# Kernel optimization log

Hardware: AMD Instinct MI355X
Metric: run time of the kernel (lower is better)

Reference implementation:

```python
import jax, jax.numpy as jnp
import numpy as np

NUM_CLASSES = 256
FEATURE_DIM = 768
BATCH = 128
SIM_BALANCE = 0.7
TIER1 = 50.0
TIER2 = 10.0
TOPK = 5


def _l2norm(x):
    return x / jnp.linalg.norm(x, axis=1, keepdims=True)


def build_edge_weights(class_features, context_features, w1, b1, w2, b2,
                       co_occurrence, instance_counts):
    """Vectorized, faithful translation of VisualFeatureGraph.build_graph."""
    N = class_features.shape[0]
    dt = class_features.dtype
    co = co_occurrence.astype(dt)            # [N,N], diag is 0
    cnt = instance_counts.astype(dt)         # [N]

    vs = _l2norm(class_features) @ _l2norm(class_features).T    # visual_sim [N,N]
    cs = _l2norm(context_features) @ _l2norm(context_features).T  # context_sim
    combined = SIM_BALANCE * vs + (1.0 - SIM_BALANCE) * cs

    # ---- Tier 1: co > TIER1 ----
    # sim_proj(f_i - f_j): exploit linearity of first layer: (f_i-f_j)@W1 = a_i - a_j
    a = class_features @ w1                                    # [N, D/2]
    h = jax.nn.relu(a[:, None, :] - a[None, :, :] + b1)        # [N,N,D/2]
    sim_weight = jax.nn.sigmoid(h @ w2 + b2)[..., 0]           # [N,N]
    ratio = (jnp.minimum(cnt[:, None], cnt[None, :]) /
             jnp.maximum(jnp.maximum(cnt[:, None], cnt[None, :]), 1.0))
    e1 = combined * sim_weight * ratio

    # ---- Tier 2: TIER2 < co <= TIER1 ----
    # shared neighbors k: co[i,k]>T1 and co[j,k]>T1 (k=i,j auto-excluded: diag=0
    # and co[i,j]<=T1 for tier-2 pairs)
    A = (co > TIER1).astype(dt)                                # [N,N]
    M = vs * A
    shared_sum = M @ M.T                                       # sum_k vs[i,k]*vs[j,k]
    shared_cnt = A @ A.T
    avg_sim = shared_sum / jnp.maximum(shared_cnt, 1.0)
    conf = co / TIER1
    e2 = jnp.where(shared_cnt > 0,
                   conf * combined + (1.0 - conf) * avg_sim,
                   conf * combined)

    # ---- Tier 3: co <= TIER2 ----
    # top-5 neighbors per row by co-occurrence among co > TIER2 (diag=0 and
    # co[i,j]<=TIER2 for tier-3 pairs, so i and j are auto-excluded)
    top_vals, top_idx = jax.lax.top_k(co, TOPK)                # [N,K]
    valid = top_vals > TIER2                                   # [N,K]
    ii = top_idx[:, None, :, None]                             # [N,1,K,1]
    jj = top_idx[None, :, None, :]                             # [1,N,1,K]
    co_cross = co[ii, jj]                                      # co[i_neigh, j_neigh] [N,N,K,K]
    vs_cross = vs[ii, jj]
    vs_in = jnp.take_along_axis(vs, top_idx, axis=1)           # vs[i, i_neigh] [N,K]
    mask = valid[:, None, :, None] & valid[None, :, None, :] & (co_cross > 0)
    w = (top_vals[:, None, :, None] * top_vals[None, :, None, :]) / TIER1
    w = jnp.where(mask, w, 0.0)
    sim = vs_in[:, None, :, None] * vs_in[None, :, None, :] * vs_cross
    trans = jnp.sum(w * sim, axis=(2, 3))                      # [N,N]
    tot = jnp.sum(w, axis=(2, 3))
    e3 = jnp.where(tot > 0, trans / jnp.where(tot > 0, tot, 1.0), 0.1 * cs)

    tier1_mask = co > TIER1
    tier2_mask = (co > TIER2) & ~tier1_mask
    E = jnp.where(tier1_mask, e1, jnp.where(tier2_mask, e2, e3))
    E = E * (1.0 - jnp.eye(N, dtype=dt))                       # i==j skipped
    mx = jnp.max(E)
    E = jnp.where(mx > 0, E / jnp.where(mx > 0, mx, 1.0), E)
    return E


def setup_inputs() -> dict:
    key = jax.random.key(0)
    ks = jax.random.split(key, 8)
    N, D, B = NUM_CLASSES, FEATURE_DIM, BATCH
    x = jax.random.normal(ks[0], (B, N, D), dtype=jnp.float32)
    class_features = jax.random.normal(ks[1], (N, D), dtype=jnp.float32) * 0.05
    context_features = jax.random.normal(ks[2], (N, D), dtype=jnp.float32) * 0.05
    w1 = jax.random.normal(ks[3], (D, D // 2), dtype=jnp.float32) * (1.0 / np.sqrt(D))
    b1 = jnp.zeros((D // 2,), dtype=jnp.float32)
    w2 = jax.random.normal(ks[4], (D // 2, 1), dtype=jnp.float32) * (1.0 / np.sqrt(D // 2))
    b2 = jnp.zeros((1,), dtype=jnp.float32)
    co = jax.random.randint(ks[5], (N, N), 0, 121, dtype=jnp.int32)
    co = (co + co.T) // 2                                      # symmetric like update_features
    co = co * (1 - jnp.eye(N, dtype=jnp.int32))                # zero diagonal
    instance_counts = jax.random.randint(ks[6], (N,), 1, 1001, dtype=jnp.int32)
    return {"x": x, "class_features": class_features,
            "context_features": context_features,
            "w1": w1, "b1": b1, "w2": w2, "b2": b2,
            "co_occurrence": co, "instance_counts": instance_counts}


def reference(x, class_features, context_features, w1, b1, w2, b2,
              co_occurrence, instance_counts):
    E = build_edge_weights(class_features, context_features, w1, b1, w2, b2,
                           co_occurrence, instance_counts)
    # torch.bmm(E.expand(B,-1,-1), x) == einsum over shared node dim
    return x + jnp.einsum('ij,bjd->bid', E, x)
```

## Files before the change

### kernel.cpp

```cpp
#include <hip/hip_runtime.h>
#include <hip/hip_bf16.h>
#include <math.h>

#define N 256
#define D 768
#define BATCH 128

typedef float f32x4 __attribute__((ext_vector_type(4)));
typedef short bf16x8 __attribute__((ext_vector_type(8)));

static __device__ __forceinline__ unsigned short f2bf(float f) {
    unsigned int u = __float_as_uint(f);
    u += 0x7fffu + ((u >> 16) & 1u);
    return (unsigned short)(u >> 16);
}
static __device__ __forceinline__ unsigned int pack2bf(float lo, float hi) {
    unsigned int a = __float_as_uint(lo);
    unsigned int b = __float_as_uint(hi);
    a += 0x7fffu + ((a >> 16) & 1u);
    b += 0x7fffu + ((b >> 16) & 1u);
    return (a >> 16) | (b & 0xffff0000u);
}

__global__ void k_stage1(const float* __restrict__ cf, const float* __restrict__ ctx,
                         float* __restrict__ vsn, float* __restrict__ csn,
                         const float* __restrict__ w1, float* __restrict__ a,
                         const int* __restrict__ co, float* __restrict__ topv,
                         int* __restrict__ topi) {
    __shared__ float sm[2 * 64 * 33];
    int bx = blockIdx.x;
    int t = threadIdx.x;
    if (bx < 512) {
        int row = bx;
        const float* src;
        float* dst;
        if (row < N) { src = cf  + row * D;       dst = vsn + row * D; }
        else         { src = ctx + (row - N) * D; dst = csn + (row - N) * D; }
        float s = 0.f;
        for (int d = t; d < D; d += 256) { float v = src[d]; s += v * v; }
        float* red = sm;
        red[t] = s; __syncthreads();
        for (int off = 128; off > 0; off >>= 1) {
            if (t < off) red[t] += red[t + off];
            __syncthreads();
        }
        float inv = 1.0f / sqrtf(red[0]);
        for (int d = t; d < D; d += 256) dst[d] = src[d] * inv;
    } else if (bx < 608) {
        int bi = bx - 512;
        int i0 = (bi / 12) * 32, j0 = (bi % 12) * 32;
        float (*Ci)[33] = (float(*)[33])sm;
        float (*Wj)[33] = (float(*)[33])(sm + 64 * 33);
        int tx = t & 15, ty = t >> 4;
        float a00 = 0.f, a01 = 0.f, a10 = 0.f, a11 = 0.f;
        for (int k0 = 0; k0 < 768; k0 += 64) {
            #pragma unroll
            for (int s = 0; s < 8; s++) {
                int idx = s * 256 + t;
                int row = idx >> 6, kc = idx & 63;
                Ci[kc][row] = cf[(i0 + row) * 768 + k0 + kc];
                int kr = idx >> 5, col = idx & 31;
                Wj[kr][col] = w1[(k0 + kr) * 384 + j0 + col];
            }
            __syncthreads();
            #pragma unroll 4
            for (int kk = 0; kk < 64; kk++) {
                float iv0 = Ci[kk][ty * 2], iv1 = Ci[kk][ty * 2 + 1];
                float jv0 = Wj[kk][tx * 2], jv1 = Wj[kk][tx * 2 + 1];
                a00 += iv0 * jv0; a01 += iv0 * jv1;
                a10 += iv1 * jv0; a11 += iv1 * jv1;
            }
            __syncthreads();
        }
        a[(i0 + ty * 2)     * 384 + j0 + tx * 2]     = a00;
        a[(i0 + ty * 2)     * 384 + j0 + tx * 2 + 1] = a01;
        a[(i0 + ty * 2 + 1) * 384 + j0 + tx * 2]     = a10;
        a[(i0 + ty * 2 + 1) * 384 + j0 + tx * 2 + 1] = a11;
    } else {
        int lane = t & 63;
        int row = (bx - 608) * 4 + (t >> 6);
        int4 v4 = *(const int4*)(co + row * 256 + lane * 4);
        int key[4];
        key[0] = v4.x * 256 + (255 - (lane * 4 + 0));
        key[1] = v4.y * 256 + (255 - (lane * 4 + 1));
        key[2] = v4.z * 256 + (255 - (lane * 4 + 2));
        key[3] = v4.w * 256 + (255 - (lane * 4 + 3));
        for (int r = 0; r < 5; r++) {
            int best = key[0];
            #pragma unroll
            for (int e = 1; e < 4; e++) best = max(best, key[e]);
            #pragma unroll
            for (int off = 32; off > 0; off >>= 1) best = max(best, __shfl_xor(best, off, 64));
            int kidx = 255 - (best & 255);
            int val = best >> 8;
            if (lane == 0) { topv[row * 5 + r] = (float)val; topi[row * 5 + r] = kidx; }
            if ((kidx >> 2) == lane) key[kidx & 3] = -1;
        }
    }
}

__global__ void k_gram2(const float* __restrict__ vsn, const float* __restrict__ csn,
                        float* __restrict__ vs, float* __restrict__ cs) {
    int bx = blockIdx.x;
    const float* S = (bx >= 64) ? csn : vsn;
    float* O       = (bx >= 64) ? cs  : vs;
    int bi = bx & 63;
    int i0 = (bi >> 3) * 32, j0 = (bi & 7) * 32;
    __shared__ float Li[64][33], Lj[64][33];
    int t = threadIdx.x;
    int tx = t & 15, ty = t >> 4;
    float a00 = 0.f, a01 = 0.f, a10 = 0.f, a11 = 0.f;
    for (int k0 = 0; k0 < 768; k0 += 64) {
        #pragma unroll
        for (int s = 0; s < 8; s++) {
            int idx = s * 256 + t;
            int row = idx >> 6, kc = idx & 63;
            Li[kc][row] = S[(i0 + row) * 768 + k0 + kc];
            Lj[kc][row] = S[(j0 + row) * 768 + k0 + kc];
        }
        __syncthreads();
        #pragma unroll 4
        for (int kk = 0; kk < 64; kk++) {
            float iv0 = Li[kk][ty * 2], iv1 = Li[kk][ty * 2 + 1];
            float jv0 = Lj[kk][tx * 2], jv1 = Lj[kk][tx * 2 + 1];
            a00 += iv0 * jv0; a01 += iv0 * jv1;
            a10 += iv1 * jv0; a11 += iv1 * jv1;
        }
        __syncthreads();
    }
    O[(i0 + ty * 2)     * 256 + j0 + tx * 2]     = a00;
    O[(i0 + ty * 2)     * 256 + j0 + tx * 2 + 1] = a01;
    O[(i0 + ty * 2 + 1) * 256 + j0 + tx * 2]     = a10;
    O[(i0 + ty * 2 + 1) * 256 + j0 + tx * 2 + 1] = a11;
}

__global__ void k_stage3(const float* __restrict__ a, const float* __restrict__ b1,
                         const float* __restrict__ w2, const float* __restrict__ b2,
                         const float* __restrict__ vs, const float* __restrict__ cs,
                         const int* __restrict__ ic, float* __restrict__ e1,
                         const int* __restrict__ co, float* __restrict__ ss,
                         float* __restrict__ sc) {
    __shared__ float sm[12800];
    int bx = blockIdx.x;
    int t = threadIdx.x;
    if (bx < 256) {
        int i0 = (bx >> 4) * 16, j0 = (bx & 15) * 16;
        float (*ai)[388]  = (float(*)[388])sm;
        float (*ajm)[388] = (float(*)[388])(sm + 16 * 388);
        float* sw2 = sm + 2 * 16 * 388;
        for (int idx = t; idx < 16 * 96; idx += 256) {
            int r = idx / 96, c = (idx % 96) * 4;
            *(float4*)&ai[r][c] = *(const float4*)(a + (i0 + r) * 384 + c);
            float4 u  = *(const float4*)(a + (j0 + r) * 384 + c);
            float4 bb = *(const float4*)(b1 + c);
            u.x -= bb.x; u.y -= bb.y; u.z -= bb.z; u.w -= bb.w;
            *(float4*)&ajm[r][c] = u;
        }
        for (int k = t; k < 384; k += 256) sw2[k] = w2[k];
        __syncthreads();
        int tx = t & 15, ty = t >> 4;
        float s = 0.f;
        #pragma unroll 4
        for (int k4 = 0; k4 < 96; k4++) {
            float4 xv = *(const float4*)&ai[ty][k4 * 4];
            float4 yv = *(const float4*)&ajm[tx][k4 * 4];
            float4 wv = *(const float4*)&sw2[k4 * 4];
            s += fmaxf(xv.x - yv.x, 0.f) * wv.x;
            s += fmaxf(xv.y - yv.y, 0.f) * wv.y;
            s += fmaxf(xv.z - yv.z, 0.f) * wv.z;
            s += fmaxf(xv.w - yv.w, 0.f) * wv.w;
        }
        int i = i0 + ty, j = j0 + tx;
        float sig = 1.0f / (1.0f + expf(-(s + b2[0])));
        float comb = 0.7f * vs[i * 256 + j] + 0.3f * cs[i * 256 + j];
        float ci = (float)ic[i], cj = (float)ic[j];
        float mn = fminf(ci, cj), mx = fmaxf(ci, cj);
        float ratio = mn / fmaxf(mx, 1.0f);
        e1[i * 256 + j] = comb * sig * ratio;
    } else {
        int bi = bx - 256;
        int i0 = (bi >> 3) * 32, j0 = (bi & 7) * 32;
        float (*Mi)[33] = (float(*)[33])sm;
        float (*Ai)[33] = (float(*)[33])(sm + 2112);
        float (*Mj)[33] = (float(*)[33])(sm + 4224);
        float (*Aj)[33] = (float(*)[33])(sm + 6336);
        int tx = t & 15, ty = t >> 4;
        float s00=0.f,s01=0.f,s10=0.f,s11=0.f;
        float c00=0.f,c01=0.f,c10=0.f,c11=0.f;
        for (int k0 = 0; k0 < 256; k0 += 64) {
            #pragma unroll
            for (int s = 0; s < 8; s++) {
                int idx = s * 256 + t;
                int row = idx >> 6, kc = idx & 63;
                int civ = co[(i0 + row) * 256 + k0 + kc];
                float aa = civ > 50 ? 1.f : 0.f;
                Ai[kc][row] = aa;
                Mi[kc][row] = aa * vs[(i0 + row) * 256 + k0 + kc];
                int cjv = co[(j0 + row) * 256 + k0 + kc];
                float ab = cjv > 50 ? 1.f : 0.f;
                Aj[kc][row] = ab;
                Mj[kc][row] = ab * vs[(j0 + row) * 256 + k0 + kc];
            }
            __syncthreads();
            #pragma unroll 4
            for (int kk = 0; kk < 64; kk++) {
                float mi0 = Mi[kk][ty*2], mi1 = Mi[kk][ty*2+1];
                float ai0 = Ai[kk][ty*2], ai1 = Ai[kk][ty*2+1];
                float mj0 = Mj[kk][tx*2], mj1 = Mj[kk][tx*2+1];
                float aj0 = Aj[kk][tx*2], aj1 = Aj[kk][tx*2+1];
                s00 += mi0*mj0; s01 += mi0*mj1; s10 += mi1*mj0; s11 += mi1*mj1;
                c00 += ai0*aj0; c01 += ai0*aj1; c10 += ai1*aj0; c11 += ai1*aj1;
            }
            __syncthreads();
        }
        ss[(i0+ty*2)  *256 + j0+tx*2]   = s00; ss[(i0+ty*2)  *256 + j0+tx*2+1] = s01;
        ss[(i0+ty*2+1)*256 + j0+tx*2]   = s10; ss[(i0+ty*2+1)*256 + j0+tx*2+1] = s11;
        sc[(i0+ty*2)  *256 + j0+tx*2]   = c00; sc[(i0+ty*2)  *256 + j0+tx*2+1] = c01;
        sc[(i0+ty*2+1)*256 + j0+tx*2]   = c10; sc[(i0+ty*2+1)*256 + j0+tx*2+1] = c11;
    }
}

__global__ void k_assemble(const int* __restrict__ co, const float* __restrict__ vs,
                           const float* __restrict__ cs, const float* __restrict__ e1,
                           const float* __restrict__ ss, const float* __restrict__ sc,
                           const float* __restrict__ topv, const int* __restrict__ topi,
                           float* __restrict__ E, float* __restrict__ partials) {
    int i = blockIdx.x, j = threadIdx.x;
    int cij = co[i * 256 + j];
    float e;
    if (i == j) {
        e = 0.f;
    } else if (cij > 50) {
        e = e1[i * 256 + j];
    } else if (cij > 10) {
        float conf = (float)cij / 50.0f;
        float comb = 0.7f * vs[i * 256 + j] + 0.3f * cs[i * 256 + j];
        float cnt = sc[i * 256 + j];
        float avg = ss[i * 256 + j] / fmaxf(cnt, 1.f);
        e = (cnt > 0.f) ? conf * comb + (1.f - conf) * avg : conf * comb;
    } else {
        float tvi[5], tvj[5]; int tii[5], tij[5];
        #pragma unroll
        for (int k = 0; k < 5; k++) {
            tvi[k] = topv[i * 5 + k]; tii[k] = topi[i * 5 + k];
            tvj[k] = topv[j * 5 + k]; tij[k] = topi[j * 5 + k];
        }
        float trans = 0.f, tot = 0.f;
        #pragma unroll
        for (int k = 0; k < 5; k++) {
            if (!(tvi[k] > 10.f)) continue;
            float vin_i = vs[i * 256 + tii[k]];
            #pragma unroll
            for (int l = 0; l < 5; l++) {
                if (!(tvj[l] > 10.f)) continue;
                int cc = co[tii[k] * 256 + tij[l]];
                if (cc <= 0) continue;
                float w = tvi[k] * tvj[l] / 50.f;
                float sim = vin_i * vs[j * 256 + tij[l]] * vs[tii[k] * 256 + tij[l]];
                trans += w * sim; tot += w;
            }
        }
        e = (tot > 0.f) ? trans / tot : 0.1f * cs[i * 256 + j];
    }
    E[i * 256 + j] = e;
    __shared__ float red[256];
    red[j] = e; __syncthreads();
    for (int off = 128; off > 0; off >>= 1) {
        if (j < off) red[j] = fmaxf(red[j], red[j + off]);
        __syncthreads();
    }
    if (j == 0) partials[i] = red[0];
}

__global__ void k_ep(const float* __restrict__ E, const float* __restrict__ partials,
                     unsigned short* __restrict__ Ep) {
    __shared__ float red[256];
    int t = threadIdx.x;
    red[t] = partials[t]; __syncthreads();
    for (int off = 128; off > 0; off >>= 1) {
        if (t < off) red[t] = fmaxf(red[t], red[t + off]);
        __syncthreads();
    }
    float mx = red[0];
    float s = (mx > 0.f) ? 1.0f / mx : 1.0f;
    int base = (blockIdx.x * 256 + t) * 4;
    float4 e4 = *(const float4*)(E + base);
    float ev[4] = {e4.x, e4.y, e4.z, e4.w};
    unsigned short o[4];
    #pragma unroll
    for (int q = 0; q < 4; q++) {
        int g = base + q;
        float v = s * ev[q] + (((g >> 8) == (g & 255)) ? 1.0f : 0.0f);
        o[q] = f2bf(v);
    }
    uint2 w;
    w.x = (unsigned int)o[0] | ((unsigned int)o[1] << 16);
    w.y = (unsigned int)o[2] | ((unsigned int)o[3] << 16);
    *(uint2*)(Ep + base) = w;
}

#define EINS_BUFB 9472

#define EIN_BODY(KT, BB, bvC, bvN)                                              \
  {                                                                             \
    _Pragma("unroll")                                                           \
    for (int s = 0; s < 4; s++) {                                               \
      uint2 pv;                                                                 \
      pv.x = pack2bf(xr[s].x, xr[s].y);                                         \
      pv.y = pack2bf(xr[s].z, xr[s].w);                                         \
      *(uint2*)((char*)xs + (BB) + wbyte + s * 32) = pv;                        \
    }                                                                           \
    __syncthreads();                                                            \
    if ((KT) < 7) {                                                             \
      const float* xn = xb + (size_t)((KT) + 1) * 32 * 768;                     \
      _Pragma("unroll")                                                         \
      for (int s = 0; s < 4; s++)                                               \
        xr[s] = *(const float4*)(xn + (size_t)(jb + s) * 768);                  \
      _Pragma("unroll")                                                         \
      for (int nf = 0; nf < 4; nf++)                                            \
        bvN[nf] = *(const uint4*)(eprow + (nf << 12) + ((KT) + 1) * 32);        \
    }                                                                           \
    uint2 a0[8], a1[8];                                                         \
    _Pragma("unroll")                                                           \
    for (int g = 0; g < 8; g++) {                                               \
      unsigned ag = ra + (BB) + g * 1184;                                       \
      asm volatile("ds_read_b64_tr_b16 %0, %1" : "=v"(a0[g]) : "v"(ag));        \
      asm volatile("ds_read_b64_tr_b16 %0, %1 offset:144" : "=v"(a1[g]) : "v"(ag)); \
    }                                                                           \
    asm volatile("s_waitcnt lgkmcnt(0)" ::: "memory");                          \
    __builtin_amdgcn_sched_barrier(0);                                          \
    _Pragma("unroll")                                                           \
    for (int mf = 0; mf < 8; mf++) {                                            \
      union { uint2 u[2]; bf16x8 v; } af;                                       \
      af.u[0] = a0[mf]; af.u[1] = a1[mf];                                       \
      _Pragma("unroll")                                                         \
      for (int nf = 0; nf < 4; nf++)                                            \
        acc[mf][nf] = __builtin_amdgcn_mfma_f32_16x16x32_bf16(                  \
            af.v, *(const bf16x8*)&bvC[nf], acc[mf][nf], 0, 0, 0);              \
    }                                                                           \
  }

__global__ __launch_bounds__(256, 2) void k_einsum_tr(
    const unsigned short* __restrict__ Ep, const float* __restrict__ x,
    float* __restrict__ out) {
    extern __shared__ unsigned short xs[];
    int t = threadIdx.x;
    int b = blockIdx.y;
    int d0 = blockIdx.x * 128;
    int lane = t & 63, w = t >> 6;
    int l15 = lane & 15, lq = lane >> 4;

    int dq = t & 31;
    int jb = (t >> 5) * 4;
    const float* xb = x + ((size_t)b * 256) * 768 + d0 + 4 * dq;
    unsigned wbyte = (unsigned)(((dq >> 2) * 592 + (jb >> 2) * 72 + (dq & 3) * 4) * 2);
    unsigned ra = (unsigned)(lq * 288 + l15 * 8);

    const unsigned short* eprow = Ep + (((w * 64 + l15) << 8) + lq * 8);

    f32x4 acc[8][4];
    #pragma unroll
    for (int mf = 0; mf < 8; mf++)
        #pragma unroll
        for (int nf = 0; nf < 4; nf++)
            #pragma unroll
            for (int e = 0; e < 4; e++) acc[mf][nf][e] = 0.f;

    float4 xr[4];
    #pragma unroll
    for (int s = 0; s < 4; s++) xr[s] = *(const float4*)(xb + (size_t)(jb + s) * 768);
    uint4 bv0[4], bv1[4];
    #pragma unroll
    for (int nf = 0; nf < 4; nf++) bv0[nf] = *(const uint4*)(eprow + (nf << 12));

    #pragma unroll
    for (int k2 = 0; k2 < 4; k2++) {
        EIN_BODY(2 * k2,     0,         bv0, bv1)
        EIN_BODY(2 * k2 + 1, EINS_BUFB, bv1, bv0)
    }

    float* ob = out + ((size_t)b * 256) * 768 + d0;
    #pragma unroll
    for (int mf = 0; mf < 8; mf++) {
        #pragma unroll
        for (int nf = 0; nf < 4; nf++) {
            int i = w * 64 + nf * 16 + l15;
            int d = mf * 16 + lq * 4;
            *(float4*)(ob + (size_t)i * 768 + d) = *(float4*)&acc[mf][nf];
        }
    }
}

extern "C" void kernel_launch(void* const* d_in, const int* in_sizes, int n_in,
                              void* d_out, int out_size, void* d_ws, size_t ws_size,
                              hipStream_t stream) {
    const float* x   = (const float*)d_in[0];
    const float* cf  = (const float*)d_in[1];
    const float* ctx = (const float*)d_in[2];
    const float* w1  = (const float*)d_in[3];
    const float* b1  = (const float*)d_in[4];
    const float* w2  = (const float*)d_in[5];
    const float* b2  = (const float*)d_in[6];
    const int*   co  = (const int*)d_in[7];
    const int*   ic  = (const int*)d_in[8];
    float* out = (float*)d_out;

    float* ws   = (float*)d_ws;
    float* vsn  = ws;
    float* csn  = vsn + 196608;
    float* a    = csn + 196608;
    float* vs   = a + 98304;
    float* cs   = vs + 65536;
    float* e1   = cs + 65536;
    float* ss   = e1 + 65536;
    float* sc   = ss + 65536;
    float* E    = sc + 65536;
    float* topv = E + 65536;
    int*   topi = (int*)(topv + 1280);
    float* partials = (float*)(topi + 1280);
    unsigned short* Ep = (unsigned short*)(partials + 256);

    k_stage1<<<672, 256, 0, stream>>>(cf, ctx, vsn, csn, w1, a, co, topv, topi);
    k_gram2<<<128, 256, 0, stream>>>(vsn, csn, vs, cs);
    k_stage3<<<320, 256, 0, stream>>>(a, b1, w2, b2, vs, cs, ic, e1, co, ss, sc);
    k_assemble<<<256, 256, 0, stream>>>(co, vs, cs, e1, ss, sc, topv, topi, E, partials);
    k_ep<<<64, 256, 0, stream>>>(E, partials, Ep);
    k_einsum_tr<<<dim3(6, BATCH), 256, 2 * EINS_BUFB, stream>>>(Ep, x, out);
}
```

Measured before the change: 290.3 us.

## Halve einsum d-tile and prefetch x two stages ahead for higher occupancy

Shrinks the einsum block tile along the feature dimension from 128 to 64, doubling the grid, and halves the shared buffers and accumulators. Launch bounds move to 3 blocks per CU. Each thread now loads a contiguous 8-float strip of x into one of two register sets, prefetching two k-steps ahead instead of one, and writes a single 16-byte packed store to LDS. The goals are more waves resident to hide memory latency and a deeper x prefetch. In exchange, each Ep tile is re-read by twice as many blocks and each MFMA block does less work per LDS read.

Result: no change. 288.2 us (-0.7%).

```diff
diff --git a/kernel.cpp b/kernel.cpp
--- a/kernel.cpp
+++ b/kernel.cpp
@@ -299,30 +299,30 @@
     *(uint2*)(Ep + base) = w;
 }
 
-#define EINS_BUFB 9472
-
-#define EIN_BODY(KT, BB, bvC, bvN)                                              \
+#define EINS_BUFB 4736
+
+#define EIN_BODY(KT, BB, XR, bvC, bvN)                                          \
   {                                                                             \
-    _Pragma("unroll")                                                           \
-    for (int s = 0; s < 4; s++) {                                               \
-      uint2 pv;                                                                 \
-      pv.x = pack2bf(xr[s].x, xr[s].y);                                         \
-      pv.y = pack2bf(xr[s].z, xr[s].w);                                         \
-      *(uint2*)((char*)xs + (BB) + wbyte + s * 32) = pv;                        \
-    }                                                                           \
+    uint4 pv;                                                                   \
+    pv.x = pack2bf(XR[0].x, XR[0].y);                                           \
+    pv.y = pack2bf(XR[0].z, XR[0].w);                                           \
+    pv.z = pack2bf(XR[1].x, XR[1].y);                                           \
+    pv.w = pack2bf(XR[1].z, XR[1].w);                                           \
+    *(uint4*)((char*)xs + (BB) + wbyte) = pv;                                   \
     __syncthreads();                                                            \
     if ((KT) < 7) {                                                             \
-      const float* xn = xb + (size_t)((KT) + 1) * 32 * 768;                     \
-      _Pragma("unroll")                                                         \
-      for (int s = 0; s < 4; s++)                                               \
-        xr[s] = *(const float4*)(xn + (size_t)(jb + s) * 768);                  \
       _Pragma("unroll")                                                         \
       for (int nf = 0; nf < 4; nf++)                                            \
         bvN[nf] = *(const uint4*)(eprow + (nf << 12) + ((KT) + 1) * 32);        \
     }                                                                           \
-    uint2 a0[8], a1[8];                                                         \
+    if ((KT) < 6) {                                                             \
+      const float* xn = xb + (size_t)((KT) + 2) * 32 * 768;                     \
+      XR[0] = *(const float4*)xn;                                               \
+      XR[1] = *(const float4*)(xn + 4);                                         \
+    }                                                                           \
+    uint2 a0[4], a1[4];                                                         \
     _Pragma("unroll")                                                           \
-    for (int g = 0; g < 8; g++) {                                               \
+    for (int g = 0; g < 4; g++) {                                               \
       unsigned ag = ra + (BB) + g * 1184;                                       \
       asm volatile("ds_read_b64_tr_b16 %0, %1" : "=v"(a0[g]) : "v"(ag));        \
       asm volatile("ds_read_b64_tr_b16 %0, %1 offset:144" : "=v"(a1[g]) : "v"(ag)); \
@@ -330,7 +330,7 @@
     asm volatile("s_waitcnt lgkmcnt(0)" ::: "memory");                          \
     __builtin_amdgcn_sched_barrier(0);                                          \
     _Pragma("unroll")                                                           \
-    for (int mf = 0; mf < 8; mf++) {                                            \
+    for (int mf = 0; mf < 4; mf++) {                                            \
       union { uint2 u[2]; bf16x8 v; } af;                                       \
       af.u[0] = a0[mf]; af.u[1] = a1[mf];                                       \
       _Pragma("unroll")                                                         \
@@ -340,48 +340,49 @@
     }                                                                           \
   }
 
-__global__ __launch_bounds__(256, 2) void k_einsum_tr(
+__global__ __launch_bounds__(256, 3) void k_einsum_tr(
     const unsigned short* __restrict__ Ep, const float* __restrict__ x,
     float* __restrict__ out) {
     extern __shared__ unsigned short xs[];
     int t = threadIdx.x;
     int b = blockIdx.y;
-    int d0 = blockIdx.x * 128;
+    int d0 = blockIdx.x * 64;
     int lane = t & 63, w = t >> 6;
     int l15 = lane & 15, lq = lane >> 4;
 
-    int dq = t & 31;
-    int jb = (t >> 5) * 4;
-    const float* xb = x + ((size_t)b * 256) * 768 + d0 + 4 * dq;
-    unsigned wbyte = (unsigned)(((dq >> 2) * 592 + (jb >> 2) * 72 + (dq & 3) * 4) * 2);
+    int dh = t & 7, kr = t >> 3;
+    const float* xb = x + ((size_t)b * 256) * 768 + (size_t)kr * 768 + d0 + dh * 8;
+    unsigned wbyte = (unsigned)((dh >> 1) * 1184 + (kr >> 2) * 144 + (kr & 3) * 32 + (dh & 1) * 16);
     unsigned ra = (unsigned)(lq * 288 + l15 * 8);
 
     const unsigned short* eprow = Ep + (((w * 64 + l15) << 8) + lq * 8);
 
-    f32x4 acc[8][4];
+    f32x4 acc[4][4];
     #pragma unroll
-    for (int mf = 0; mf < 8; mf++)
+    for (int mf = 0; mf < 4; mf++)
         #pragma unroll
         for (int nf = 0; nf < 4; nf++)
             #pragma unroll
             for (int e = 0; e < 4; e++) acc[mf][nf][e] = 0.f;
 
-    float4 xr[4];
-    #pragma unroll
-    for (int s = 0; s < 4; s++) xr[s] = *(const float4*)(xb + (size_t)(jb + s) * 768);
+    float4 xA[2], xB[2];
+    xA[0] = *(const float4*)xb;
+    xA[1] = *(const float4*)(xb + 4);
+    xB[0] = *(const float4*)(xb + 32 * 768);
+    xB[1] = *(const float4*)(xb + 32 * 768 + 4);
     uint4 bv0[4], bv1[4];
     #pragma unroll
     for (int nf = 0; nf < 4; nf++) bv0[nf] = *(const uint4*)(eprow + (nf << 12));
 
     #pragma unroll
     for (int k2 = 0; k2 < 4; k2++) {
-        EIN_BODY(2 * k2,     0,         bv0, bv1)
-        EIN_BODY(2 * k2 + 1, EINS_BUFB, bv1, bv0)
+        EIN_BODY(2 * k2,     0,         xA, bv0, bv1)
+        EIN_BODY(2 * k2 + 1, EINS_BUFB, xB, bv1, bv0)
     }
 
     float* ob = out + ((size_t)b * 256) * 768 + d0;
     #pragma unroll
-    for (int mf = 0; mf < 8; mf++) {
+    for (int mf = 0; mf < 4; mf++) {
         #pragma unroll
         for (int nf = 0; nf < 4; nf++) {
             int i = w * 64 + nf * 16 + l15;
@@ -425,5 +426,5 @@
     k_stage3<<<320, 256, 0, stream>>>(a, b1, w2, b2, vs, cs, ic, e1, co, ss, sc);
     k_assemble<<<256, 256, 0, stream>>>(co, vs, cs, e1, ss, sc, topv, topi, E, partials);
     k_ep<<<64, 256, 0, stream>>>(E, partials, Ep);
-    k_einsum_tr<<<dim3(6, BATCH), 256, 2 * EINS_BUFB, stream>>>(Ep, x, out);
-}
+    k_einsum_tr<<<dim3(12, BATCH), 256, 2 * EINS_BUFB, stream>>>(Ep, x, out);
+}
```
